# Kernel tuning notes

Hardware: AMD Instinct MI355X
Metric: run time of the kernel (lower is better)

Reference implementation:

```python
import jax, jax.numpy as jnp
import numpy as np

B, S, D = 16, 2048, 1024  # batch, max_len, inp_size == hidden_size


def setup_inputs() -> dict:
    key = jax.random.key(0)
    k1, k2, k3, k4, k5, k6 = jax.random.split(key, 6)
    stdv = 1.0 / np.sqrt(D)
    return {
        "encoder_outputs": jax.random.normal(k1, (B, S, D), dtype=jnp.float32),
        "hidden": jax.random.normal(k2, (B, D), dtype=jnp.float32),
        "lengths": jax.random.randint(k3, (B,), 1, S + 1, dtype=jnp.int32),
        "W": jax.random.normal(k4, (D, 2 * D), dtype=jnp.float32) * stdv,
        "b": jax.random.normal(k5, (D,), dtype=jnp.float32) * stdv,
        "v": jax.random.normal(k6, (D,), dtype=jnp.float32) * stdv,
    }


def reference(encoder_outputs, hidden, lengths, W, b, v):
    # Linear on cat([H, enc]) == H @ Wh^T + enc @ We^T + b (avoids materializing the concat)
    Wh, We = W[:, :D], W[:, D:]              # [D_out, D] each
    hid_proj = hidden @ Wh.T                  # [B, D]
    enc_proj = jnp.einsum('bsd,ed->bse', encoder_outputs, We)  # [B, S, D]
    energy = jnp.tanh(enc_proj + hid_proj[:, None, :] + b)     # [B, S, D]
    scores = jnp.einsum('bsd,d->bs', energy, v)                # [B, S]
    # mask positions >= length to -inf before softmax
    valid = jnp.arange(S)[None, :] < lengths[:, None]          # [B, S]
    scores = jnp.where(valid, scores, -jnp.inf)
    attn = jax.nn.softmax(scores, axis=-1)                     # [B, S]
    context = jnp.einsum('bs,bsd->bd', attn, encoder_outputs)  # [B, D]
    return context[:, None, :]                                 # [B, 1, D] to match torch bmm output
```

## Files before the change

### kernel.cpp

```cpp
#include <hip/hip_runtime.h>
#include <cstdint>

#define DEV static __device__ __forceinline__

typedef __attribute__((__ext_vector_type__(8))) __bf16 bf16x8;
typedef __attribute__((__ext_vector_type__(4))) float f32x4;

static constexpr int Bc = 16, Sc = 2048, Dc = 1024;

DEV unsigned short f2bf(float x) {
  unsigned int u = __float_as_uint(x);
  unsigned int r = (u + 0x7fffu + ((u >> 16) & 1u)) >> 16;
  return (unsigned short)r;
}
DEV unsigned int pack2(float a, float b) {
  return (unsigned int)f2bf(a) | ((unsigned int)f2bf(b) << 16);
}
DEV float tanh_fast(float x) {
  return 1.f - 2.f / (__expf(2.f * x) + 1.f);
}
DEV void gload16(const void* g, void* l) {
  __builtin_amdgcn_global_load_lds(
      (const __attribute__((address_space(1))) unsigned int*)g,
      (__attribute__((address_space(3))) unsigned int*)l, 16, 0, 0);
}

__global__ __launch_bounds__(256) void k_prep(const float* __restrict__ enc,
                                              const float* __restrict__ hidden,
                                              const float* __restrict__ W,
                                              const float* __restrict__ bias,
                                              const int* __restrict__ lengths,
                                              unsigned short* __restrict__ ebf,
                                              unsigned short* __restrict__ webf,
                                              float* __restrict__ hp,
                                              int* __restrict__ wl) {
  int bx = blockIdx.x;
  int t = threadIdx.x;
  if (bx < 2048) {
    int team = t >> 7, lane = t & 127;
    int r0 = bx * 16;
    int b = r0 >> 11;
    int len = lengths[b];
    for (int rr = team; rr < 16; rr += 2) {
      int s = (r0 + rr) & 2047;
      if (s >= len) continue;
      const float* src = enc + (size_t)(r0 + rr) * Dc + lane * 8;
      unsigned short* dst = ebf + (size_t)(r0 + rr) * Dc + lane * 8;
      float4 f0 = *(const float4*)src;
      float4 f1 = *(const float4*)(src + 4);
      uint4 o;
      o.x = pack2(f0.x, f0.y);
      o.y = pack2(f0.z, f0.w);
      o.z = pack2(f1.x, f1.y);
      o.w = pack2(f1.z, f1.w);
      *(uint4*)dst = o;
    }
  } else if (bx < 3072) {
    int e = bx - 2048;
    if (e == 0) {
      int sblk = t >> 4, b = t & 15;
      int active = (sblk * 128 < lengths[b]) ? 1 : 0;
      unsigned long long mask = __ballot(active);
      int lane = t & 63, wid = t >> 6;
      int prefix = __popcll(mask & ((1ull << lane) - 1ull));
      __shared__ int woff[4];
      if (lane == 0) woff[wid] = __popcll(mask);
      __syncthreads();
      int base = 0;
      for (int i = 0; i < wid; i++) base += woff[i];
      if (active) wl[1 + base + prefix] = (b << 8) | sblk;
      if (t == 0) wl[0] = woff[0] + woff[1] + woff[2] + woff[3];
    }
    __shared__ float wrow[Dc];
    for (int i = t; i < Dc; i += 256) wrow[i] = W[(size_t)e * 2048 + i];
    __syncthreads();
    int w = t >> 6, lane = t & 63;
    float bv = bias[e];
    for (int bi = w; bi < Bc; bi += 4) {
      float s = 0.f;
      const float* hrow = hidden + (size_t)bi * Dc;
      for (int d = lane; d < Dc; d += 64) s += hrow[d] * wrow[d];
      for (int m = 1; m < 64; m <<= 1) s += __shfl_xor(s, m);
      if (lane == 0) hp[(size_t)bi * Dc + e] = s + bv;
    }
  } else {
    int i = ((bx - 3072) * 256 + t) * 8;
    int e = i >> 10, d = i & 1023;
    const float* p = W + (size_t)e * 2048 + 1024 + d;
    float4 f0 = *(const float4*)p;
    float4 f1 = *(const float4*)(p + 4);
    uint4 o;
    o.x = pack2(f0.x, f0.y);
    o.y = pack2(f0.z, f0.w);
    o.z = pack2(f1.x, f1.y);
    o.w = pack2(f1.z, f1.w);
    *(uint4*)(webf + i) = o;
  }
}

__global__ __launch_bounds__(256) void k_scores(const unsigned short* __restrict__ Ae,
                                                const unsigned short* __restrict__ We,
                                                const float* __restrict__ hp,
                                                const float* __restrict__ v,
                                                const int* __restrict__ wl,
                                                float* __restrict__ pscores) {
  int g = blockIdx.x & 255;
  int et = blockIdx.x >> 8;
  if (g >= wl[0]) return;
  int pk = wl[1 + g];
  int b = pk >> 8, sblk = pk & 255;
  int s0 = sblk * 128;
  int m0 = b * Sc + s0;
  int e0 = et * 128;

  __shared__ unsigned short As0[128 * 32];
  __shared__ unsigned short As1[128 * 32];
  __shared__ unsigned short Bs0[128 * 32];
  __shared__ unsigned short Bs1[128 * 32];
  __shared__ float hp_s[128], v_s[128], sc_s[128];

  int t = threadIdx.x;
  int w = t >> 6, lane = t & 63;
  if (t < 128) {
    hp_s[t] = hp[(size_t)b * Dc + e0 + t];
    v_s[t] = v[e0 + t];
    sc_s[t] = 0.f;
  }
  asm volatile("s_waitcnt vmcnt(0) lgkmcnt(0)" ::: "memory");

  f32x4 acc[4][4] = {};
  int wr = w >> 1, wc = w & 1;

  {
    int o = t >> 3, q = t & 7;
    int g8 = q ^ (o & 7);
    int srow = 2 * o + (g8 >> 2);
    int scol = (g8 & 3) * 8;
    Ae += (size_t)(m0 + srow) * Dc + scol;
    We += (size_t)(e0 + srow) * Dc + scol;
  }
  const unsigned short* ga0 = Ae;
  const unsigned short* gb0 = We;

  int posw = (((lane & 1) << 2) + (lane >> 4)) ^ (((lane & 15) >> 1) & 7);
  int aoff = (wr * 32 + ((lane & 15) >> 1)) * 64 + posw * 8;
  int boff = (wc * 32 + ((lane & 15) >> 1)) * 64 + posw * 8;

  auto stage = [&](int k0, unsigned short* A, unsigned short* B) {
    gload16(ga0 + k0, A + w * 512);
    gload16(ga0 + k0 + 64 * Dc, A + 2048 + w * 512);
    gload16(gb0 + k0, B + w * 512);
    gload16(gb0 + k0 + 64 * Dc, B + 2048 + w * 512);
  };
  auto compute = [&](const unsigned short* A, const unsigned short* B) {
    bf16x8 af[4], bfr[4];
#pragma unroll
    for (int m = 0; m < 4; m++)
      af[m] = __builtin_bit_cast(bf16x8, *(const uint4*)(A + aoff + m * 512));
#pragma unroll
    for (int n = 0; n < 4; n++)
      bfr[n] = __builtin_bit_cast(bf16x8, *(const uint4*)(B + boff + n * 512));
    __builtin_amdgcn_s_setprio(1);
#pragma unroll
    for (int m = 0; m < 4; m++)
#pragma unroll
      for (int n = 0; n < 4; n++)
        acc[m][n] = __builtin_amdgcn_mfma_f32_16x16x32_bf16(af[m], bfr[n], acc[m][n], 0, 0, 0);
    __builtin_amdgcn_s_setprio(0);
  };

  stage(0, As0, Bs0);

#pragma unroll 1
  for (int i2 = 0; i2 < 15; ++i2) {
    stage((2 * i2 + 1) * 32, As1, Bs1);
    asm volatile("s_waitcnt vmcnt(4)" ::: "memory");
    __builtin_amdgcn_sched_barrier(0);
    __builtin_amdgcn_s_barrier();
    __builtin_amdgcn_sched_barrier(0);
    compute(As0, Bs0);
    __builtin_amdgcn_sched_barrier(0);
    __builtin_amdgcn_s_barrier();
    stage((2 * i2 + 2) * 32, As0, Bs0);
    asm volatile("s_waitcnt vmcnt(4)" ::: "memory");
    __builtin_amdgcn_sched_barrier(0);
    __builtin_amdgcn_s_barrier();
    __builtin_amdgcn_sched_barrier(0);
    compute(As1, Bs1);
    __builtin_amdgcn_sched_barrier(0);
    __builtin_amdgcn_s_barrier();
  }
  stage(31 * 32, As1, Bs1);
  asm volatile("s_waitcnt vmcnt(4)" ::: "memory");
  __builtin_amdgcn_sched_barrier(0);
  __builtin_amdgcn_s_barrier();
  __builtin_amdgcn_sched_barrier(0);
  compute(As0, Bs0);
  __builtin_amdgcn_sched_barrier(0);
  __builtin_amdgcn_s_barrier();
  asm volatile("s_waitcnt vmcnt(0)" ::: "memory");
  __builtin_amdgcn_sched_barrier(0);
  __builtin_amdgcn_s_barrier();
  __builtin_amdgcn_sched_barrier(0);
  compute(As1, Bs1);

  for (int m = 0; m < 4; m++) {
    float rs0 = 0.f, rs1 = 0.f, rs2 = 0.f, rs3 = 0.f;
    for (int n = 0; n < 4; n++) {
      int ec = wc * 64 + n * 16 + (lane & 15);
      float hpv = hp_s[ec], vv = v_s[ec];
      f32x4 a = acc[m][n];
      rs0 += vv * tanh_fast(a[0] + hpv);
      rs1 += vv * tanh_fast(a[1] + hpv);
      rs2 += vv * tanh_fast(a[2] + hpv);
      rs3 += vv * tanh_fast(a[3] + hpv);
    }
    for (int mask = 1; mask < 16; mask <<= 1) {
      rs0 += __shfl_xor(rs0, mask);
      rs1 += __shfl_xor(rs1, mask);
      rs2 += __shfl_xor(rs2, mask);
      rs3 += __shfl_xor(rs3, mask);
    }
    if ((lane & 15) == 0) {
      int rbase = wr * 64 + m * 16 + (lane >> 4) * 4;
      atomicAdd(&sc_s[rbase + 0], rs0);
      atomicAdd(&sc_s[rbase + 1], rs1);
      atomicAdd(&sc_s[rbase + 2], rs2);
      atomicAdd(&sc_s[rbase + 3], rs3);
    }
  }
  __syncthreads();
  if (t < 128) pscores[((size_t)et * Bc + b) * Sc + s0 + t] = sc_s[t];
}

__global__ __launch_bounds__(256) void k_softmax(const float* __restrict__ pscores,
                                                 const int* __restrict__ lengths,
                                                 float* __restrict__ attn) {
  int b = blockIdx.x, t = threadIdx.x;
  int len = lengths[b];
  float vals[8];
  float mx = -INFINITY;
  for (int i = 0; i < 8; i++) {
    int s = t + i * 256;
    float sc = 0.f;
    for (int p = 0; p < 8; p++) sc += pscores[((size_t)p * Bc + b) * Sc + s];
    sc = (s < len) ? sc : -INFINITY;
    vals[i] = sc;
    mx = fmaxf(mx, sc);
  }
  for (int m = 1; m < 64; m <<= 1) mx = fmaxf(mx, __shfl_xor(mx, m));
  __shared__ float rmax[4], rsum[4];
  int w = t >> 6, lane = t & 63;
  if (lane == 0) rmax[w] = mx;
  __syncthreads();
  mx = fmaxf(fmaxf(rmax[0], rmax[1]), fmaxf(rmax[2], rmax[3]));
  float sm = 0.f;
  for (int i = 0; i < 8; i++) {
    vals[i] = __expf(vals[i] - mx);
    sm += vals[i];
  }
  for (int m = 1; m < 64; m <<= 1) sm += __shfl_xor(sm, m);
  if (lane == 0) rsum[w] = sm;
  __syncthreads();
  sm = rsum[0] + rsum[1] + rsum[2] + rsum[3];
  float inv = 1.f / sm;
  for (int i = 0; i < 8; i++) attn[(size_t)b * Sc + t + i * 256] = vals[i] * inv;
}

__global__ __launch_bounds__(256) void k_ctx(const unsigned short* __restrict__ ebf,
                                             const float* __restrict__ attn,
                                             const int* __restrict__ lengths,
                                             float* __restrict__ pctx) {
  int b = blockIdx.x >> 4, sp = blockIdx.x & 15;
  int t = threadIdx.x;
  int d0 = t * 4;
  int sbeg = sp * 128;
  float* outp = pctx + ((size_t)sp * Bc + b) * Dc + d0;
  int len = lengths[b];
  if (sbeg >= len) {
    *(float4*)outp = make_float4(0.f, 0.f, 0.f, 0.f);
    return;
  }
  __shared__ float at_s[128];
  if (t < 128) at_s[t] = attn[(size_t)b * Sc + sbeg + t];
  __syncthreads();
  float4 a = make_float4(0.f, 0.f, 0.f, 0.f);
  const unsigned short* ebase = ebf + ((size_t)b * Sc + sbeg) * Dc + d0;
  int ns = min(128, len - sbeg);
  for (int i = 0; i < ns; i++) {
    float wt = at_s[i];
    uint2 u = *(const uint2*)(ebase + (size_t)i * Dc);
    a.x += wt * __uint_as_float(u.x << 16);
    a.y += wt * __uint_as_float(u.x & 0xffff0000u);
    a.z += wt * __uint_as_float(u.y << 16);
    a.w += wt * __uint_as_float(u.y & 0xffff0000u);
  }
  *(float4*)outp = a;
}

__global__ __launch_bounds__(256) void k_reduce(const float* __restrict__ pctx,
                                               float* __restrict__ out) {
  int i = blockIdx.x * 256 + threadIdx.x;
  int b = i >> 10, d = i & 1023;
  float s = 0.f;
  for (int p = 0; p < 16; p++) s += pctx[((size_t)p * Bc + b) * Dc + d];
  out[i] = s;
}

extern "C" void kernel_launch(void* const* d_in, const int* in_sizes, int n_in,
                              void* d_out, int out_size, void* d_ws, size_t ws_size,
                              hipStream_t stream) {
  const float* enc = (const float*)d_in[0];
  const float* hidden = (const float*)d_in[1];
  const int* lengths = (const int*)d_in[2];
  const float* W = (const float*)d_in[3];
  const float* bias = (const float*)d_in[4];
  const float* v = (const float*)d_in[5];
  float* out = (float*)d_out;

  char* ws = (char*)d_ws;
  unsigned short* ebf = (unsigned short*)ws;
  unsigned short* webf = (unsigned short*)(ws + 67108864);
  float* hp = (float*)(ws + 69206016);
  float* pscores = (float*)(ws + 69271552);
  float* attn = (float*)(ws + 70320128);
  float* pctx = (float*)(ws + 70451200);
  int* wl = (int*)(ws + 71499776);

  hipLaunchKernelGGL(k_prep, dim3(3584), dim3(256), 0, stream, enc, hidden, W, bias,
                     lengths, ebf, webf, hp, wl);
  hipLaunchKernelGGL(k_scores, dim3(2048), dim3(256), 0, stream, ebf, webf, hp, v,
                     wl, pscores);
  hipLaunchKernelGGL(k_softmax, dim3(16), dim3(256), 0, stream, pscores, lengths, attn);
  hipLaunchKernelGGL(k_ctx, dim3(256), dim3(256), 0, stream, ebf, attn, lengths, pctx);
  hipLaunchKernelGGL(k_reduce, dim3(64), dim3(256), 0, stream, pctx, out);
}
```

Before: 95.32 us.

## Fuse context reduction into k_ctx by splitting dims across blocks

Restructures the context kernel so each block owns 64 output dimensions of one batch and its four wavefronts split the valid sequence range, reducing partials in shared memory and writing the final output directly. This removes the separate reduction kernel and the partial-context workspace round trip. In exchange, loads become scalar 16-bit per lane instead of 8-byte vector loads, and the attention weights are read from global memory per step rather than staged in LDS, which may lower memory efficiency.

```diff
diff --git a/kernel.cpp b/kernel.cpp
--- a/kernel.cpp
+++ b/kernel.cpp
@@ -270,41 +270,34 @@
 __global__ __launch_bounds__(256) void k_ctx(const unsigned short* __restrict__ ebf,
                                              const float* __restrict__ attn,
                                              const int* __restrict__ lengths,
-                                             float* __restrict__ pctx) {
-  int b = blockIdx.x >> 4, sp = blockIdx.x & 15;
+                                             float* __restrict__ out) {
+  int b = blockIdx.x >> 4, ch = blockIdx.x & 15;
   int t = threadIdx.x;
-  int d0 = t * 4;
-  int sbeg = sp * 128;
-  float* outp = pctx + ((size_t)sp * Bc + b) * Dc + d0;
+  int q = t >> 6, lane = t & 63;
+  int d = ch * 64 + lane;
   int len = lengths[b];
-  if (sbeg >= len) {
-    *(float4*)outp = make_float4(0.f, 0.f, 0.f, 0.f);
-    return;
-  }
-  __shared__ float at_s[128];
-  if (t < 128) at_s[t] = attn[(size_t)b * Sc + sbeg + t];
+  int len4 = (len + 3) >> 2;
+  int sbeg = q * len4;
+  int send = min(sbeg + len4, len);
+  float acc0 = 0.f, acc1 = 0.f;
+  const unsigned short* ebase = ebf + (size_t)b * Sc * Dc + d;
+  const float* abase = attn + (size_t)b * Sc;
+  int s = sbeg;
+  for (; s + 1 < send; s += 2) {
+    float w0 = abase[s], w1 = abase[s + 1];
+    float e0 = __uint_as_float((unsigned int)ebase[(size_t)s * Dc] << 16);
+    float e1 = __uint_as_float((unsigned int)ebase[(size_t)(s + 1) * Dc] << 16);
+    acc0 += w0 * e0;
+    acc1 += w1 * e1;
+  }
+  if (s < send)
+    acc0 += abase[s] * __uint_as_float((unsigned int)ebase[(size_t)s * Dc] << 16);
+  __shared__ float part[4][64];
+  part[q][lane] = acc0 + acc1;
   __syncthreads();
-  float4 a = make_float4(0.f, 0.f, 0.f, 0.f);
-  const unsigned short* ebase = ebf + ((size_t)b * Sc + sbeg) * Dc + d0;
-  int ns = min(128, len - sbeg);
-  for (int i = 0; i < ns; i++) {
-    float wt = at_s[i];
-    uint2 u = *(const uint2*)(ebase + (size_t)i * Dc);
-    a.x += wt * __uint_as_float(u.x << 16);
-    a.y += wt * __uint_as_float(u.x & 0xffff0000u);
-    a.z += wt * __uint_as_float(u.y << 16);
-    a.w += wt * __uint_as_float(u.y & 0xffff0000u);
-  }
-  *(float4*)outp = a;
-}
-
-__global__ __launch_bounds__(256) void k_reduce(const float* __restrict__ pctx,
-                                               float* __restrict__ out) {
-  int i = blockIdx.x * 256 + threadIdx.x;
-  int b = i >> 10, d = i & 1023;
-  float s = 0.f;
-  for (int p = 0; p < 16; p++) s += pctx[((size_t)p * Bc + b) * Dc + d];
-  out[i] = s;
+  if (t < 64)
+    out[(size_t)b * Dc + ch * 64 + t] =
+        part[0][t] + part[1][t] + part[2][t] + part[3][t];
 }
 
 extern "C" void kernel_launch(void* const* d_in, const int* in_sizes, int n_in,
@@ -324,14 +317,12 @@
   float* hp = (float*)(ws + 69206016);
   float* pscores = (float*)(ws + 69271552);
   float* attn = (float*)(ws + 70320128);
-  float* pctx = (float*)(ws + 70451200);
-  int* wl = (int*)(ws + 71499776);
+  int* wl = (int*)(ws + 70451200);
 
   hipLaunchKernelGGL(k_prep, dim3(3584), dim3(256), 0, stream, enc, hidden, W, bias,
                      lengths, ebf, webf, hp, wl);
   hipLaunchKernelGGL(k_scores, dim3(2048), dim3(256), 0, stream, ebf, webf, hp, v,
                      wl, pscores);
   hipLaunchKernelGGL(k_softmax, dim3(16), dim3(256), 0, stream, pscores, lengths, attn);
-  hipLaunchKernelGGL(k_ctx, dim3(256), dim3(256), 0, stream, ebf, attn, lengths, pctx);
-  hipLaunchKernelGGL(k_reduce, dim3(64), dim3(256), 0, stream, pctx, out);
-}
+  hipLaunchKernelGGL(k_ctx, dim3(256), dim3(256), 0, stream, ebf, attn, lengths, out);
+}
```

New measurement: 154.3 us. 1.62x slower.
